# Optimization experiments

Measured on AMD Instinct MI355X. Metric: run time of the kernel, lower is better.

Reference implementation:

```python
import jax, jax.numpy as jnp
import numpy as np

N = 50000      # num nodes
E = 1_600_000  # num edges (avg degree 32)
L = 200_000    # num label edges to decode
D_IN, H1, H2 = 256, 128, 64


def setup_inputs() -> dict:
    key = jax.random.key(0)
    ks = jax.random.split(key, 20)

    def w(k, fan_in, fan_out):
        return jax.random.normal(k, (fan_in, fan_out), jnp.float32) * (1.0 / np.sqrt(fan_in))

    return {
        'x': jax.random.normal(ks[0], (N, D_IN), jnp.float32),
        'prev0': jax.random.normal(ks[1], (N, H1), jnp.float32),
        'prev1': jax.random.normal(ks[2], (N, H2), jnp.float32),
        'Wpre1': w(ks[3], D_IN, 256), 'bpre1': jnp.zeros((256,), jnp.float32),
        'Wpre2': w(ks[4], 256, 128),  'bpre2': jnp.zeros((128,), jnp.float32),
        'Wc1': w(ks[5], 128, H1),     'bc1': jnp.zeros((H1,), jnp.float32),
        'Wc2': w(ks[6], H1, H2),      'bc2': jnp.zeros((H2,), jnp.float32),
        'Wm1': w(ks[7], 2 * H1, H1),  'bm1': jnp.zeros((H1,), jnp.float32),
        'Wm2': w(ks[8], 2 * H2, H2),  'bm2': jnp.zeros((H2,), jnp.float32),
        'Wpost': w(ks[9], H2, 2),     'bpost': jnp.zeros((2,), jnp.float32),
        'edge_index': jax.random.randint(ks[10], (2, E), 0, N, jnp.int32),
        'edge_label_index': jax.random.randint(ks[11], (2, L), 0, N, jnp.int32),
    }


def _gcn_conv(h, W, b, src, dst, n):
    """PyG GCNConv: add self-loops, sym-normalize D^-1/2 (A+I) D^-1/2 (X W) + b."""
    hw = h @ W                                   # [N, out]
    deg = jax.ops.segment_sum(jnp.ones_like(src, jnp.float32), dst, num_segments=n) + 1.0
    dinv = jax.lax.rsqrt(deg)                    # [N]
    norm = dinv[src] * dinv[dst]                 # [E]
    agg = jax.ops.segment_sum(hw[src] * norm[:, None], dst, num_segments=n)
    agg = agg + hw * (dinv * dinv)[:, None]      # self-loop term
    return agg + b


def reference(x, prev0, prev1, Wpre1, bpre1, Wpre2, bpre2, Wc1, bc1, Wc2, bc2,
              Wm1, bm1, Wm2, bm2, Wpost, bpost, edge_index, edge_label_index):
    # isnap > 0 with update='mlp'; dropout p=0.0 -> identity
    src, dst = edge_index[0], edge_index[1]
    n = x.shape[0]

    h = jax.nn.relu(x @ Wpre1 + bpre1)
    h = jax.nn.relu(h @ Wpre2 + bpre2)

    h = jax.nn.relu(_gcn_conv(h, Wc1, bc1, src, dst, n))
    h = jnp.concatenate([h, prev0], axis=1) @ Wm1 + bm1   # temporal MLP update 1
    emb0 = h

    h = jax.nn.relu(_gcn_conv(h, Wc2, bc2, src, dst, n))
    h = jnp.concatenate([h, prev1], axis=1) @ Wm2 + bm2   # temporal MLP update 2
    emb1 = h

    # hadamard edge decode
    h_had = emb1[edge_label_index[0]] * emb1[edge_label_index[1]]  # [L, H2]
    pred = jnp.sum(h_had @ Wpost + bpost, axis=-1)                 # [L]
    return pred, emb0, emb1
```

## Files before the change

### kernel.cpp

```cpp
#include <hip/hip_runtime.h>
#include <hip/hip_bf16.h>


typedef unsigned short ushort_t;
typedef __attribute__((ext_vector_type(8))) short s8v;
typedef __attribute__((ext_vector_type(4))) float f4;

#define BSHIFT 8

__device__ __forceinline__ ushort_t f2bf(float v) {
    unsigned u = __float_as_uint(v);
    return (ushort_t)((u + 0x7FFFu + ((u >> 16) & 1u)) >> 16);
}

__device__ __forceinline__ s8v cvt8(f4 v0, f4 v1) {
    ushort_t hb[8];
    hb[0] = f2bf(v0.x); hb[1] = f2bf(v0.y); hb[2] = f2bf(v0.z); hb[3] = f2bf(v0.w);
    hb[4] = f2bf(v1.x); hb[5] = f2bf(v1.y); hb[6] = f2bf(v1.z); hb[7] = f2bf(v1.w);
    return *(s8v*)hb;
}

__device__ __forceinline__ void dma16(const ushort_t* g, ushort_t* l) {
    __builtin_amdgcn_global_load_lds(
        (const __attribute__((address_space(1))) unsigned int*)g,
        (__attribute__((address_space(3))) unsigned int*)l, 16, 0, 0);
}

__global__ __launch_bounds__(256) void f2b_kernel(const float* __restrict__ in,
                                                  ushort_t* __restrict__ out, size_t n) {
    size_t i = ((size_t)blockIdx.x * 256 + threadIdx.x) * 8;
    if (i + 8 > n) return;
    f4 v0 = *(const f4*)&in[i];
    f4 v1 = *(const f4*)&in[i + 4];
    *(s8v*)&out[i] = cvt8(v0, v1);
}

template <int BN, int KW, int K1, bool A1F32, bool RELU, bool SCALE, bool DUAL, int OUTMODE>
__global__ __launch_bounds__(256, 2) void gemm_lds(
    const float* __restrict__ A1f, const ushort_t* __restrict__ A1h,
    const ushort_t* __restrict__ A2h,
    const ushort_t* __restrict__ Wt,
    const float* __restrict__ bias, const float* __restrict__ rowscale,
    float* __restrict__ Cf, ushort_t* __restrict__ Ch,
    int M, int Nout)
{
    constexpr int NT = BN / 32;
    constexpr int K2 = KW - K1;
    __shared__ ushort_t Abuf[128 * 64];
    __shared__ ushort_t Bbuf[BN * 64];

    const int tid  = threadIdx.x;
    const int lane = tid & 63;
    const int w    = tid >> 6;
    const int wr   = w >> 1, wc = w & 1;
    const int rbase = blockIdx.y * 128;
    const int bn    = blockIdx.x * BN;

    f4 acc[4][NT];
    const f4 zero = {0.f, 0.f, 0.f, 0.f};
#pragma unroll
    for (int mi = 0; mi < 4; ++mi)
#pragma unroll
        for (int ni = 0; ni < NT; ++ni) acc[mi][ni] = zero;

    for (int kt = 0; kt < KW; kt += 64) {
        if constexpr (A1F32) {
#pragma unroll
            for (int j = 0; j < 4; ++j) {
                const int c2 = tid + j * 256;
                const int row = c2 >> 3, c = c2 & 7;
                const int gr = min(rbase + row, M - 1);
                const float* p = &A1f[(size_t)gr * K1 + kt + c * 8];
                *(s8v*)&Abuf[row * 64 + c * 8] = cvt8(*(const f4*)p, *(const f4*)(p + 4));
            }
        } else {
#pragma unroll
            for (int i = 0; i < 4; ++i) {
                const int s = w * 4 + i;
                const int row = s * 8 + (lane >> 3);
                const int c = lane & 7;
                const int gr = min(rbase + row, M - 1);
                const ushort_t* g;
                if (DUAL && kt >= K1) g = &A2h[(size_t)gr * K2 + (kt - K1) + c * 8];
                else                  g = &A1h[(size_t)gr * K1 + kt + c * 8];
                dma16(g, &Abuf[s * 512]);
            }
        }
#pragma unroll
        for (int i = 0; i < NT; ++i) {
            const int s = w * NT + i;
            const int colr = s * 8 + (lane >> 3);
            const int c = lane & 7;
            const ushort_t* g = &Wt[(size_t)(bn + colr) * KW + kt + c * 8];
            dma16(g, &Bbuf[s * 512]);
        }
        __syncthreads();
#pragma unroll
        for (int ks = 0; ks < 2; ++ks) {
            s8v bfrag[NT];
#pragma unroll
            for (int ni = 0; ni < NT; ++ni) {
                const int col = wc * (NT * 16) + ni * 16 + (lane & 15);
                bfrag[ni] = *(const s8v*)&Bbuf[col * 64 + ks * 32 + (lane >> 4) * 8];
            }
#pragma unroll
            for (int mi = 0; mi < 4; ++mi) {
                const int row = wr * 64 + mi * 16 + (lane & 15);
                const s8v af = *(const s8v*)&Abuf[row * 64 + ks * 32 + (lane >> 4) * 8];
#pragma unroll
                for (int ni = 0; ni < NT; ++ni)
                    acc[mi][ni] = __builtin_amdgcn_mfma_f32_16x16x32_bf16(af, bfrag[ni], acc[mi][ni], 0, 0, 0);
            }
        }
        __syncthreads();
    }

#pragma unroll
    for (int mi = 0; mi < 4; ++mi) {
#pragma unroll
        for (int reg = 0; reg < 4; ++reg) {
            const int row = rbase + wr * 64 + mi * 16 + (lane >> 4) * 4 + reg;
            if (row >= M) continue;
            const float rs = SCALE ? rowscale[row] : 1.f;
#pragma unroll
            for (int ni = 0; ni < NT; ++ni) {
                const int col = bn + wc * (NT * 16) + ni * 16 + (lane & 15);
                float v = acc[mi][ni][reg];
                if (SCALE) v *= rs;
                if (bias) v += bias[col];
                if (RELU) v = fmaxf(v, 0.f);
                if constexpr (OUTMODE == 2) {
                    Ch[(size_t)row * Nout + col] = f2bf(v);
                } else if constexpr (OUTMODE == 3) {
                    Cf[(size_t)row * Nout + col] = v;
                    Ch[(size_t)row * Nout + col] = f2bf(v);
                } else {
                    Cf[(size_t)row * Nout + col] = v;
                }
            }
        }
    }
}

struct WDesc { const float* W; ushort_t* h; int K; int No; };
struct WAll { WDesc d[6]; };

__global__ void wtcvt_kernel(WAll wa) {
    WDesc d = wa.d[blockIdx.y];
    int e = blockIdx.x * blockDim.x + threadIdx.x;
    if (e >= d.K * d.No) return;
    int k = e / d.No, n = e - k * d.No;
    d.h[(size_t)n * d.K + k] = f2bf(d.W[e]);
}

__global__ __launch_bounds__(256) void bcount_kernel(const int* __restrict__ dst,
                                                     int* __restrict__ bcount, int E, int NB) {
    __shared__ int cnt[256];
    const int t = threadIdx.x;
    if (t < NB) cnt[t] = 0;
    __syncthreads();
    for (int e = blockIdx.x * 256 + t; e < E; e += gridDim.x * 256)
        atomicAdd(&cnt[dst[e] >> BSHIFT], 1);
    __syncthreads();
    if (t < NB && cnt[t]) atomicAdd(&bcount[t], cnt[t]);
}

__global__ __launch_bounds__(256) void bscan_kernel(const int* __restrict__ bcount,
                                                    int* __restrict__ bbase,
                                                    int* __restrict__ bcursor, int NB, int E) {
    __shared__ int s[256];
    const int t = threadIdx.x;
    s[t] = (t < NB) ? bcount[t] : 0;
    __syncthreads();
    for (int off = 1; off < 256; off <<= 1) {
        int v = (t >= off) ? s[t - off] : 0;
        __syncthreads();
        s[t] += v;
        __syncthreads();
    }
    int excl = t ? s[t - 1] : 0;
    if (t < NB) { bbase[t] = excl; bcursor[t] = excl; }
    if (t == 0) bbase[NB] = E;
}

__global__ __launch_bounds__(256) void bpart_kernel(const int* __restrict__ src,
                                                    const int* __restrict__ dst,
                                                    int* __restrict__ bcursor,
                                                    unsigned* __restrict__ packed, int E, int NB) {
    __shared__ int cnt[256];
    __shared__ int cur[256];
    const int t = threadIdx.x;
    const int beg = blockIdx.x * 8192;
    const int end = min(beg + 8192, E);
    if (t < NB) cnt[t] = 0;
    __syncthreads();
    for (int e = beg + t; e < end; e += 256) atomicAdd(&cnt[dst[e] >> BSHIFT], 1);
    __syncthreads();
    if (t < NB && cnt[t]) cur[t] = atomicAdd(&bcursor[t], cnt[t]);
    __syncthreads();
    for (int e = beg + t; e < end; e += 256) {
        int d = dst[e];
        int b = d >> BSHIFT;
        int pos = atomicAdd(&cur[b], 1);
        packed[pos] = (unsigned)src[e] | ((unsigned)(d & ((1 << BSHIFT) - 1)) << 16);
    }
}

__global__ __launch_bounds__(256) void bbuild_kernel(const int* __restrict__ bbase,
                                                     const unsigned* __restrict__ packed,
                                                     int* __restrict__ col,
                                                     int* __restrict__ rowstart,
                                                     float* __restrict__ dinv, int N, int E) {
    __shared__ int ncnt[256];
    __shared__ int s[256];
    __shared__ int ncur[256];
    const int b = blockIdx.x;
    const int t = threadIdx.x;
    const int beg = bbase[b], end = bbase[b + 1];
    const int node0 = b << BSHIFT;
    const int nInB = min(256, N - node0);
    ncnt[t] = 0;
    __syncthreads();
    for (int e = beg + t; e < end; e += 256) atomicAdd(&ncnt[packed[e] >> 16], 1);
    __syncthreads();
    s[t] = ncnt[t];
    __syncthreads();
    for (int off = 1; off < 256; off <<= 1) {
        int v = (t >= off) ? s[t - off] : 0;
        __syncthreads();
        s[t] += v;
        __syncthreads();
    }
    int excl = t ? s[t - 1] : 0;
    if (t < nInB) {
        rowstart[node0 + t] = beg + excl;
        dinv[node0 + t] = rsqrtf((float)ncnt[t] + 1.0f);
    }
    ncur[t] = beg + excl;
    __syncthreads();
    for (int e = beg + t; e < end; e += 256) {
        unsigned p = packed[e];
        int pos = atomicAdd(&ncur[p >> 16], 1);
        col[pos] = (int)(p & 0xFFFFu);
    }
    if (b == 0 && t == 0) rowstart[N] = E;
}

template <int F>
__global__ __launch_bounds__(256) void gather_bf_kernel(const int* __restrict__ rowstart,
                                                        const int* __restrict__ col,
                                                        const float* __restrict__ dinv,
                                                        const ushort_t* __restrict__ hws,
                                                        const float* __restrict__ bias,
                                                        ushort_t* __restrict__ aggb, int N) {
    const int wave = threadIdx.x >> 6;
    const int lane = threadIdx.x & 63;
    const int d = blockIdx.x * 4 + wave;
    if (d >= N) return;
    const int beg = rowstart[d], end = rowstart[d + 1];
    const float dd = dinv[d];
    if (F == 128) {
        const unsigned* base = (const unsigned*)hws;
        unsigned sv = base[(size_t)d * 64 + lane];
        float ax = __uint_as_float(sv << 16);
        float ay = __uint_as_float(sv & 0xFFFF0000u);
        for (int e0 = beg; e0 < end; e0 += 64) {
            int nid = (e0 + lane < end) ? col[e0 + lane] : 0;
            int cnt = min(64, end - e0);
            int j = 0;
            for (; j + 8 <= cnt; j += 8) {
                unsigned u[8];
#pragma unroll
                for (int q = 0; q < 8; ++q) {
                    int s = __shfl(nid, j + q);
                    u[q] = base[(size_t)s * 64 + lane];
                }
#pragma unroll
                for (int q = 0; q < 8; ++q) {
                    ax += __uint_as_float(u[q] << 16);
                    ay += __uint_as_float(u[q] & 0xFFFF0000u);
                }
            }
            for (; j < cnt; ++j) {
                int s = __shfl(nid, j);
                unsigned uu = base[(size_t)s * 64 + lane];
                ax += __uint_as_float(uu << 16);
                ay += __uint_as_float(uu & 0xFFFF0000u);
            }
        }
        float2 b = ((const float2*)bias)[lane];
        float rx = fmaxf(ax * dd + b.x, 0.f);
        float ry = fmaxf(ay * dd + b.y, 0.f);
        unsigned pk = ((unsigned)f2bf(ry) << 16) | (unsigned)f2bf(rx);
        ((unsigned*)aggb)[(size_t)d * 64 + lane] = pk;
    } else {
        float acc = __uint_as_float((unsigned)hws[(size_t)d * 64 + lane] << 16);
        for (int e0 = beg; e0 < end; e0 += 64) {
            int nid = (e0 + lane < end) ? col[e0 + lane] : 0;
            int cnt = min(64, end - e0);
            int j = 0;
            for (; j + 8 <= cnt; j += 8) {
                ushort_t u[8];
#pragma unroll
                for (int q = 0; q < 8; ++q) {
                    int s = __shfl(nid, j + q);
                    u[q] = hws[(size_t)s * 64 + lane];
                }
#pragma unroll
                for (int q = 0; q < 8; ++q) acc += __uint_as_float((unsigned)u[q] << 16);
            }
            for (; j < cnt; ++j) {
                int s = __shfl(nid, j);
                acc += __uint_as_float((unsigned)hws[(size_t)s * 64 + lane] << 16);
            }
        }
        acc = fmaxf(acc * dd + bias[lane], 0.f);
        aggb[(size_t)d * 64 + lane] = f2bf(acc);
    }
}

__global__ __launch_bounds__(256) void decode_kernel(const ushort_t* __restrict__ emb1b,
                                                     const int* __restrict__ eli,
                                                     const float* __restrict__ Wpost,
                                                     const float* __restrict__ bpost,
                                                     float* __restrict__ pred, int L) {
    const int wave = threadIdx.x >> 6;
    const int lane = threadIdx.x & 63;
    const int l = blockIdx.x * 4 + wave;
    if (l >= L) return;
    int s = eli[l];
    int d = eli[L + l];
    float w = Wpost[lane * 2] + Wpost[lane * 2 + 1];
    float a = __uint_as_float((unsigned)emb1b[(size_t)s * 64 + lane] << 16);
    float b = __uint_as_float((unsigned)emb1b[(size_t)d * 64 + lane] << 16);
    float p = a * b * w;
#pragma unroll
    for (int off = 32; off; off >>= 1) p += __shfl_down(p, off);
    if (lane == 0) pred[l] = p + bpost[0] + bpost[1];
}

extern "C" void kernel_launch(void* const* d_in, const int* in_sizes, int n_in,
                              void* d_out, int out_size, void* d_ws, size_t ws_size,
                              hipStream_t stream) {
    const float* x     = (const float*)d_in[0];
    const float* prev0 = (const float*)d_in[1];
    const float* prev1 = (const float*)d_in[2];
    const float* Wpre1 = (const float*)d_in[3];
    const float* bpre1 = (const float*)d_in[4];
    const float* Wpre2 = (const float*)d_in[5];
    const float* bpre2 = (const float*)d_in[6];
    const float* Wc1   = (const float*)d_in[7];
    const float* bc1   = (const float*)d_in[8];
    const float* Wc2   = (const float*)d_in[9];
    const float* bc2   = (const float*)d_in[10];
    const float* Wm1   = (const float*)d_in[11];
    const float* bm1   = (const float*)d_in[12];
    const float* Wm2   = (const float*)d_in[13];
    const float* bm2   = (const float*)d_in[14];
    const float* Wpost = (const float*)d_in[15];
    const float* bpost = (const float*)d_in[16];
    const int* edge_index = (const int*)d_in[17];
    const int* eli        = (const int*)d_in[18];

    const int N = in_sizes[0] / 256;
    const int E = in_sizes[17] / 2;
    const int L = in_sizes[18] / 2;
    const int NB = (N + 255) >> BSHIFT;

    const int* src = edge_index;
    const int* dst = edge_index + E;

    float* out  = (float*)d_out;
    float* pred = out;
    float* emb0 = out + L;
    float* emb1 = out + L + (size_t)N * 128;

    float* ws = (float*)d_ws;
    unsigned* packed = (unsigned*)ws;
    ushort_t* h1h   = (ushort_t*)ws;
    ushort_t* hws1b = (ushort_t*)ws;
    ushort_t* emb0b = (ushort_t*)ws;
    ushort_t* emb1b = (ushort_t*)ws;
    ushort_t* agg1b = (ushort_t*)(ws + (size_t)64 * N);
    ushort_t* hws2b = (ushort_t*)(ws + (size_t)64 * N);
    ushort_t* agg2b = (ushort_t*)(ws + (size_t)96 * N);
    ushort_t* h2b   = (ushort_t*)(ws + (size_t)128 * N);
    ushort_t* p0b   = (ushort_t*)(ws + (size_t)192 * N);
    ushort_t* p1b   = (ushort_t*)(ws + (size_t)256 * N);
    int*      col   = (int*)(ws + (size_t)288 * N);

    size_t o = (size_t)320 * N;
    int* rowstart = (int*)(ws + o);         o += ((size_t)N + 4) & ~(size_t)3;
    float* dinv = ws + o;                   o += ((size_t)N + 3) & ~(size_t)3;
    int* bbase = (int*)(ws + o);            o += 260;
    int* bcursor = (int*)(ws + o);          o += 260;
    int* bcount = (int*)(ws + o);           o += 260;
    ushort_t* wb = (ushort_t*)(ws + o);

    ushort_t* wpre1t = wb + 0;
    ushort_t* wpre2t = wb + 65536;
    ushort_t* wc1t   = wb + 98304;
    ushort_t* wm1t   = wb + 114688;
    ushort_t* wc2t   = wb + 147456;
    ushort_t* wm2t   = wb + 155648;

    {
        size_t n0 = (size_t)N * 128, n1 = (size_t)N * 64;
        f2b_kernel<<<(int)((n0 / 8 + 255) / 256), 256, 0, stream>>>(prev0, p0b, n0);
        f2b_kernel<<<(int)((n1 / 8 + 255) / 256), 256, 0, stream>>>(prev1, p1b, n1);
    }

    hipMemsetAsync(bcount, 0, (size_t)NB * sizeof(int), stream);
    bcount_kernel<<<1024, 256, 0, stream>>>(dst, bcount, E, NB);
    bscan_kernel<<<1, 256, 0, stream>>>(bcount, bbase, bcursor, NB, E);
    bpart_kernel<<<(E + 8191) / 8192, 256, 0, stream>>>(src, dst, bcursor, packed, E, NB);
    bbuild_kernel<<<NB, 256, 0, stream>>>(bbase, packed, col, rowstart, dinv, N, E);

    WAll wa;
    wa.d[0] = {Wpre1, wpre1t, 256, 256};
    wa.d[1] = {Wpre2, wpre2t, 256, 128};
    wa.d[2] = {Wc1,   wc1t,   128, 128};
    wa.d[3] = {Wm1,   wm1t,   256, 128};
    wa.d[4] = {Wc2,   wc2t,   128, 64};
    wa.d[5] = {Wm2,   wm2t,   128, 64};
    wtcvt_kernel<<<dim3(256, 6), 256, 0, stream>>>(wa);

    const int gy = (N + 127) / 128;

    gemm_lds<128, 256, 256, true, true, false, false, 2><<<dim3(2, gy), 256, 0, stream>>>(
        x, nullptr, nullptr, wpre1t, bpre1, nullptr, nullptr, h1h, N, 256);
    gemm_lds<128, 256, 256, false, true, false, false, 2><<<dim3(1, gy), 256, 0, stream>>>(
        nullptr, h1h, nullptr, wpre2t, bpre2, nullptr, nullptr, h2b, N, 128);
    gemm_lds<128, 128, 128, false, false, true, false, 2><<<dim3(1, gy), 256, 0, stream>>>(
        nullptr, h2b, nullptr, wc1t, nullptr, dinv, nullptr, hws1b, N, 128);
    gather_bf_kernel<128><<<(N + 3) / 4, 256, 0, stream>>>(rowstart, col, dinv, hws1b, bc1, agg1b, N);
    gemm_lds<128, 256, 128, false, false, false, true, 3><<<dim3(1, gy), 256, 0, stream>>>(
        nullptr, agg1b, p0b, wm1t, bm1, nullptr, emb0, emb0b, N, 128);
    gemm_lds<64, 128, 128, false, false, true, false, 2><<<dim3(1, gy), 256, 0, stream>>>(
        nullptr, emb0b, nullptr, wc2t, nullptr, dinv, nullptr, hws2b, N, 64);
    gather_bf_kernel<64><<<(N + 3) / 4, 256, 0, stream>>>(rowstart, col, dinv, hws2b, bc2, agg2b, N);
    gemm_lds<64, 128, 64, false, false, false, true, 3><<<dim3(1, gy), 256, 0, stream>>>(
        nullptr, agg2b, p1b, wm2t, bm2, nullptr, emb1, emb1b, N, 64);
    decode_kernel<<<(L + 3) / 4, 256, 0, stream>>>(emb1b, eli, Wpost, bpost, pred, L);
}
```

Before: 327.5 us.

## Swizzle bf16 operand layouts for conflict-free LDS reads and double-buffer GEMM tiles

Producers of GEMM A-operands (f32->bf16 conversion, GEMM epilogues, gather kernels) and the weight transpose now write bf16 data with an XOR swizzle of 16-byte chunks within each 64-wide k-block. The direct global-to-LDS DMA therefore lands data in a bank-conflict-free pattern, and the MFMA fragment reads use the matching swizzled index. The GEMM also double-buffers LDS tiles, prefetching the next k-tile (through registers for the f32 input) while computing the current one. This is meant to cut LDS bank conflicts and hide load latency, at the cost of twice the LDS use, which may reduce occupancy, and a layout contract that every producer and consumer must follow.

Result: slower. 342.8 us (+4.7%).

```diff
diff --git a/kernel.cpp b/kernel.cpp
--- a/kernel.cpp
+++ b/kernel.cpp
@@ -20,22 +20,30 @@
     return *(s8v*)hb;
 }
 
+__device__ __forceinline__ size_t swzidx(int row, int k, int Wd) {
+    int p = (((k & 63) >> 3) ^ (row & 7));
+    return (size_t)row * Wd + (k & ~63) + p * 8 + (k & 7);
+}
+
 __device__ __forceinline__ void dma16(const ushort_t* g, ushort_t* l) {
     __builtin_amdgcn_global_load_lds(
         (const __attribute__((address_space(1))) unsigned int*)g,
         (__attribute__((address_space(3))) unsigned int*)l, 16, 0, 0);
 }
 
-__global__ __launch_bounds__(256) void f2b_kernel(const float* __restrict__ in,
-                                                  ushort_t* __restrict__ out, size_t n) {
+template <int W>
+__global__ __launch_bounds__(256) void f2bswz_kernel(const float* __restrict__ in,
+                                                     ushort_t* __restrict__ out, size_t n) {
     size_t i = ((size_t)blockIdx.x * 256 + threadIdx.x) * 8;
     if (i + 8 > n) return;
     f4 v0 = *(const f4*)&in[i];
     f4 v1 = *(const f4*)&in[i + 4];
-    *(s8v*)&out[i] = cvt8(v0, v1);
-}
-
-template <int BN, int KW, int K1, bool A1F32, bool RELU, bool SCALE, bool DUAL, int OUTMODE>
+    int row = (int)(i / W), k = (int)(i % W);
+    *(s8v*)&out[swzidx(row, k, W)] = cvt8(v0, v1);
+}
+
+template <int BN, int KW, int K1, bool A1F32, bool RELU, bool SCALE, bool DUAL,
+          int OUTMODE, bool SWZO>
 __global__ __launch_bounds__(256, 2) void gemm_lds(
     const float* __restrict__ A1f, const ushort_t* __restrict__ A1h,
     const ushort_t* __restrict__ A2h,
@@ -46,8 +54,9 @@
 {
     constexpr int NT = BN / 32;
     constexpr int K2 = KW - K1;
-    __shared__ ushort_t Abuf[128 * 64];
-    __shared__ ushort_t Bbuf[BN * 64];
+    constexpr int NTILE = KW / 64;
+    __shared__ ushort_t Abuf[2][128 * 64];
+    __shared__ ushort_t Bbuf[2][BN * 64];
 
     const int tid  = threadIdx.x;
     const int lane = tid & 63;
@@ -63,55 +72,82 @@
 #pragma unroll
         for (int ni = 0; ni < NT; ++ni) acc[mi][ni] = zero;
 
-    for (int kt = 0; kt < KW; kt += 64) {
-        if constexpr (A1F32) {
-#pragma unroll
-            for (int j = 0; j < 4; ++j) {
-                const int c2 = tid + j * 256;
-                const int row = c2 >> 3, c = c2 & 7;
-                const int gr = min(rbase + row, M - 1);
-                const float* p = &A1f[(size_t)gr * K1 + kt + c * 8];
-                *(s8v*)&Abuf[row * 64 + c * 8] = cvt8(*(const f4*)p, *(const f4*)(p + 4));
-            }
-        } else {
-#pragma unroll
-            for (int i = 0; i < 4; ++i) {
-                const int s = w * 4 + i;
-                const int row = s * 8 + (lane >> 3);
-                const int c = lane & 7;
-                const int gr = min(rbase + row, M - 1);
-                const ushort_t* g;
-                if (DUAL && kt >= K1) g = &A2h[(size_t)gr * K2 + (kt - K1) + c * 8];
-                else                  g = &A1h[(size_t)gr * K1 + kt + c * 8];
-                dma16(g, &Abuf[s * 512]);
-            }
-        }
+    f4 pr[8];
+
+    auto gloadF32 = [&](int kt) {
+#pragma unroll
+        for (int j = 0; j < 4; ++j) {
+            const int c2 = tid + j * 256;
+            const int row = c2 >> 3, c = c2 & 7;
+            const int gr = min(rbase + row, M - 1);
+            const float* p = &A1f[(size_t)gr * K1 + kt + c * 8];
+            pr[2 * j] = *(const f4*)p;
+            pr[2 * j + 1] = *(const f4*)(p + 4);
+        }
+    };
+    auto dswriteF32 = [&](int buf) {
+#pragma unroll
+        for (int j = 0; j < 4; ++j) {
+            const int c2 = tid + j * 256;
+            const int row = c2 >> 3, c = c2 & 7;
+            const int pc = c ^ (row & 7);
+            *(s8v*)&Abuf[buf][row * 64 + pc * 8] = cvt8(pr[2 * j], pr[2 * j + 1]);
+        }
+    };
+    auto stageA = [&](int buf, int kt) {
+#pragma unroll
+        for (int i = 0; i < 4; ++i) {
+            const int s = w * 4 + i;
+            const int row = s * 8 + (lane >> 3);
+            const int c = lane & 7;
+            const int gr = min(rbase + row, M - 1);
+            const ushort_t* g;
+            if (DUAL && kt >= K1) g = &A2h[(size_t)gr * K2 + (kt - K1) + c * 8];
+            else                  g = &A1h[(size_t)gr * K1 + kt + c * 8];
+            dma16(g, &Abuf[buf][s * 512]);
+        }
+    };
+    auto stageB = [&](int buf, int kt) {
 #pragma unroll
         for (int i = 0; i < NT; ++i) {
             const int s = w * NT + i;
             const int colr = s * 8 + (lane >> 3);
             const int c = lane & 7;
-            const ushort_t* g = &Wt[(size_t)(bn + colr) * KW + kt + c * 8];
-            dma16(g, &Bbuf[s * 512]);
-        }
-        __syncthreads();
+            dma16(&Wt[(size_t)(bn + colr) * KW + kt + c * 8], &Bbuf[buf][s * 512]);
+        }
+    };
+
+    if constexpr (A1F32) { gloadF32(0); dswriteF32(0); }
+    else                 { stageA(0, 0); }
+    stageB(0, 0);
+    __syncthreads();
+
+    for (int t = 0; t < NTILE; ++t) {
+        const int cur = t & 1;
+        if (t + 1 < NTILE) {
+            if constexpr (A1F32) gloadF32((t + 1) * 64);
+            else                 stageA(cur ^ 1, (t + 1) * 64);
+            stageB(cur ^ 1, (t + 1) * 64);
+        }
 #pragma unroll
         for (int ks = 0; ks < 2; ++ks) {
+            const int c = ks * 4 + (lane >> 4);
             s8v bfrag[NT];
 #pragma unroll
             for (int ni = 0; ni < NT; ++ni) {
-                const int col = wc * (NT * 16) + ni * 16 + (lane & 15);
-                bfrag[ni] = *(const s8v*)&Bbuf[col * 64 + ks * 32 + (lane >> 4) * 8];
+                const int colr = wc * (NT * 16) + ni * 16 + (lane & 15);
+                bfrag[ni] = *(const s8v*)&Bbuf[cur][colr * 64 + (c ^ (colr & 7)) * 8];
             }
 #pragma unroll
             for (int mi = 0; mi < 4; ++mi) {
                 const int row = wr * 64 + mi * 16 + (lane & 15);
-                const s8v af = *(const s8v*)&Abuf[row * 64 + ks * 32 + (lane >> 4) * 8];
+                const s8v af = *(const s8v*)&Abuf[cur][row * 64 + (c ^ (row & 7)) * 8];
 #pragma unroll
                 for (int ni = 0; ni < NT; ++ni)
                     acc[mi][ni] = __builtin_amdgcn_mfma_f32_16x16x32_bf16(af, bfrag[ni], acc[mi][ni], 0, 0, 0);
             }
         }
+        if constexpr (A1F32) { if (t + 1 < NTILE) dswriteF32(cur ^ 1); }
         __syncthreads();
     }
 
@@ -129,11 +165,12 @@
                 if (SCALE) v *= rs;
                 if (bias) v += bias[col];
                 if (RELU) v = fmaxf(v, 0.f);
+                const size_t oidx = SWZO ? swzidx(row, col, Nout) : ((size_t)row * Nout + col);
                 if constexpr (OUTMODE == 2) {
-                    Ch[(size_t)row * Nout + col] = f2bf(v);
+                    Ch[oidx] = f2bf(v);
                 } else if constexpr (OUTMODE == 3) {
                     Cf[(size_t)row * Nout + col] = v;
-                    Ch[(size_t)row * Nout + col] = f2bf(v);
+                    Ch[oidx] = f2bf(v);
                 } else {
                     Cf[(size_t)row * Nout + col] = v;
                 }
@@ -150,7 +187,7 @@
     int e = blockIdx.x * blockDim.x + threadIdx.x;
     if (e >= d.K * d.No) return;
     int k = e / d.No, n = e - k * d.No;
-    d.h[(size_t)n * d.K + k] = f2bf(d.W[e]);
+    d.h[swzidx(n, k, d.K)] = f2bf(d.W[e]);
 }
 
 __global__ __launch_bounds__(256) void bcount_kernel(const int* __restrict__ dst,
@@ -292,7 +329,9 @@
         float rx = fmaxf(ax * dd + b.x, 0.f);
         float ry = fmaxf(ay * dd + b.y, 0.f);
         unsigned pk = ((unsigned)f2bf(ry) << 16) | (unsigned)f2bf(rx);
-        ((unsigned*)aggb)[(size_t)d * 64 + lane] = pk;
+        const int p = ((lane >> 2) & 7) ^ (d & 7);
+        const int uidx = (lane >> 5) * 32 + p * 4 + (lane & 3);
+        ((unsigned*)aggb)[(size_t)d * 64 + uidx] = pk;
     } else {
         float acc = __uint_as_float((unsigned)hws[(size_t)d * 64 + lane] << 16);
         for (int e0 = beg; e0 < end; e0 += 64) {
@@ -315,7 +354,8 @@
             }
         }
         acc = fmaxf(acc * dd + bias[lane], 0.f);
-        aggb[(size_t)d * 64 + lane] = f2bf(acc);
+        const int p = (lane >> 3) ^ (d & 7);
+        aggb[(size_t)d * 64 + p * 8 + (lane & 7)] = f2bf(acc);
     }
 }
 
@@ -406,8 +446,8 @@
 
     {
         size_t n0 = (size_t)N * 128, n1 = (size_t)N * 64;
-        f2b_kernel<<<(int)((n0 / 8 + 255) / 256), 256, 0, stream>>>(prev0, p0b, n0);
-        f2b_kernel<<<(int)((n1 / 8 + 255) / 256), 256, 0, stream>>>(prev1, p1b, n1);
+        f2bswz_kernel<128><<<(int)((n0 / 8 + 255) / 256), 256, 0, stream>>>(prev0, p0b, n0);
+        f2bswz_kernel<64><<<(int)((n1 / 8 + 255) / 256), 256, 0, stream>>>(prev1, p1b, n1);
     }
 
     hipMemsetAsync(bcount, 0, (size_t)NB * sizeof(int), stream);
@@ -427,19 +467,19 @@
 
     const int gy = (N + 127) / 128;
 
-    gemm_lds<128, 256, 256, true, true, false, false, 2><<<dim3(2, gy), 256, 0, stream>>>(
+    gemm_lds<128, 256, 256, true, true, false, false, 2, true><<<dim3(2, gy), 256, 0, stream>>>(
         x, nullptr, nullptr, wpre1t, bpre1, nullptr, nullptr, h1h, N, 256);
-    gemm_lds<128, 256, 256, false, true, false, false, 2><<<dim3(1, gy), 256, 0, stream>>>(
+    gemm_lds<128, 256, 256, false, true, false, false, 2, true><<<dim3(1, gy), 256, 0, stream>>>(
         nullptr, h1h, nullptr, wpre2t, bpre2, nullptr, nullptr, h2b, N, 128);
-    gemm_lds<128, 128, 128, false, false, true, false, 2><<<dim3(1, gy), 256, 0, stream>>>(
+    gemm_lds<128, 128, 128, false, false, true, false, 2, false><<<dim3(1, gy), 256, 0, stream>>>(
         nullptr, h2b, nullptr, wc1t, nullptr, dinv, nullptr, hws1b, N, 128);
     gather_bf_kernel<128><<<(N + 3) / 4, 256, 0, stream>>>(rowstart, col, dinv, hws1b, bc1, agg1b, N);
-    gemm_lds<128, 256, 128, false, false, false, true, 3><<<dim3(1, gy), 256, 0, stream>>>(
+    gemm_lds<128, 256, 128, false, false, false, true, 3, true><<<dim3(1, gy), 256, 0, stream>>>(
         nullptr, agg1b, p0b, wm1t, bm1, nullptr, emb0, emb0b, N, 128);
-    gemm_lds<64, 128, 128, false, false, true, false, 2><<<dim3(1, gy), 256, 0, stream>>>(
+    gemm_lds<64, 128, 128, false, false, true, false, 2, false><<<dim3(1, gy), 256, 0, stream>>>(
         nullptr, emb0b, nullptr, wc2t, nullptr, dinv, nullptr, hws2b, N, 64);
     gather_bf_kernel<64><<<(N + 3) / 4, 256, 0, stream>>>(rowstart, col, dinv, hws2b, bc2, agg2b, N);
-    gemm_lds<64, 128, 64, false, false, false, true, 3><<<dim3(1, gy), 256, 0, stream>>>(
+    gemm_lds<64, 128, 64, false, false, false, true, 3, false><<<dim3(1, gy), 256, 0, stream>>>(
         nullptr, agg2b, p1b, wm2t, bm2, nullptr, emb1, emb1b, N, 64);
     decode_kernel<<<(L + 3) / 4, 256, 0, stream>>>(emb1b, eli, Wpost, bpost, pred, L);
 }
```
